# Kernel optimization log

Hardware: AMD Instinct MI355X
Metric: run time of the kernel (lower is better)

Reference implementation:

```python
import jax, jax.numpy as jnp
import numpy as np

N_NODES = 100000
N_EDGES = 400000  # per edge type
N_ETYPES = 3
N_LAYERS = 3      # 1 + (n_layers-1) + 1 with n_layers=2
D = 64


def setup_inputs() -> dict:
    key = jax.random.key(0)
    k1, k2, k3, k4, k5 = jax.random.split(key, 5)
    feat = jax.random.normal(k1, (N_NODES, D), dtype=jnp.float32)
    # SAGEConv weights per (layer, etype): fc_self, fc_neigh, bias
    W_self = jax.random.normal(k2, (N_LAYERS, N_ETYPES, D, D), dtype=jnp.float32) * 0.05
    W_neigh = jax.random.normal(k3, (N_LAYERS, N_ETYPES, D, D), dtype=jnp.float32) * 0.05
    b = jnp.zeros((N_LAYERS, N_ETYPES, D), dtype=jnp.float32)
    src = jax.random.randint(k4, (N_ETYPES, N_EDGES), 0, N_NODES, dtype=jnp.int32)
    dst = jax.random.randint(k5, (N_ETYPES, N_EDGES), 0, N_NODES, dtype=jnp.int32)
    return {"feat": feat, "W_self": W_self, "W_neigh": W_neigh, "b": b,
            "src": src, "dst": dst}


def reference(feat, W_self, W_neigh, b, src, dst):
    # Heterogeneous SAGEConv (mean aggregator) + cross-relation sum, 3 layers.
    N = feat.shape[0]
    L, T = W_self.shape[0], W_self.shape[1]
    E = src.shape[1]
    ones = jnp.ones((E,), dtype=feat.dtype)
    h = feat
    for l in range(L):
        apply_act = l < L - 1  # last layer has no activation
        out = jnp.zeros((N, W_self.shape[-1]), dtype=feat.dtype)
        for t in range(T):  # small fixed set of relation types
            msgs = jnp.take(h, src[t], axis=0)                    # [E, d] gather
            agg = jax.ops.segment_sum(msgs, dst[t], num_segments=N)   # [N, d]
            deg = jax.ops.segment_sum(ones, dst[t], num_segments=N)   # [N]
            mean = agg / jnp.maximum(deg, 1.0)[:, None]           # zero-deg -> 0
            r = h @ W_self[l, t] + mean @ W_neigh[l, t] + b[l, t]
            if apply_act:
                r = jax.nn.relu(r)
            out = out + r  # HeteroGraphConv aggregate='sum'
        h = out
    return h
```

## Files before the change

kernel.cpp:

```cpp
#include <hip/hip_runtime.h>
#include <hip/hip_bf16.h>

#define NN 100000
#define NE 400000
#define NT 3
#define NL 3
#define DD 64
#define M_TOT (NT * NN)
#define RPB 2048
#define NBKT ((M_TOT + RPB - 1) / RPB)
#define P3CAP 32
#define P3GRID 256
#define PCAP 13312
#define CSR_THREADS 1024
#define COLCAP_BKT 9216
#define OVF_CAP 500000


typedef __attribute__((ext_vector_type(8))) short bf16x8;
typedef __attribute__((ext_vector_type(4))) float f32x4;

static __device__ __forceinline__ unsigned short f2b(float f) {
    __hip_bfloat16 b = __float2bfloat16(f);
    return *reinterpret_cast<unsigned short*>(&b);
}
static __device__ __forceinline__ float b2f(unsigned short u) {
    __hip_bfloat16 b = *reinterpret_cast<__hip_bfloat16*>(&u);
    return __bfloat162float(b);
}

__global__ void init_kernel(int* __restrict__ gcur, int* __restrict__ ocnt) {
    int i = threadIdx.x;
    if (i < NBKT) gcur[i] = i * PCAP;
    if (i == 0) ocnt[0] = 0;
}

__global__ __launch_bounds__(256) void pair_scatter(
    const int* __restrict__ src, const int* __restrict__ dst,
    int* __restrict__ gcur, unsigned* __restrict__ pairs,
    uint2* __restrict__ ovf, int* __restrict__ ocnt) {
    __shared__ unsigned buf[NBKT][P3CAP];
    __shared__ int fill[NBKT];
    for (int i = threadIdx.x; i < NBKT; i += 256) fill[i] = 0;
    __syncthreads();
    const int total = NT * NE;
    int per = (total + gridDim.x - 1) / gridDim.x;
    int beg = blockIdx.x * per;
    int fin = beg + per; if (fin > total) fin = total;
    for (int bse = beg; bse < fin; bse += 256) {
        int e = bse + threadIdx.x;
        if (e < fin) {
            int t = e / NE;
            int row = t * NN + dst[e];
            int bk = row >> 11;
            unsigned pr = ((unsigned)(row & 2047) << 17) | (unsigned)src[e];
            int pos = atomicAdd(&fill[bk], 1);
            if (pos < P3CAP) buf[bk][pos] = pr;
            else {
                int o = atomicAdd(ocnt, 1);
                if (o < OVF_CAP) ovf[o] = make_uint2((unsigned)src[e], (unsigned)row);
            }
        }
        __syncthreads();
        for (int bk = threadIdx.x; bk < NBKT; bk += 256) {
            int n = fill[bk]; if (n > P3CAP) n = P3CAP;
            int g = n >> 4;
            if (g) {
                int gb = atomicAdd(&gcur[bk], g * 16);
#pragma unroll
                for (int q = 0; q < 4; ++q)
                    *(int4*)&pairs[gb + q * 4] = *(const int4*)&buf[bk][q * 4];
                if (g == 2)
#pragma unroll
                    for (int q = 0; q < 4; ++q)
                        *(int4*)&pairs[gb + 16 + q * 4] =
                            *(const int4*)&buf[bk][16 + q * 4];
                int rem = n - g * 16;
                for (int k = 0; k < rem; ++k) buf[bk][k] = buf[bk][g * 16 + k];
                fill[bk] = rem;
            } else fill[bk] = n;
        }
        __syncthreads();
    }
    for (int bk = threadIdx.x; bk < NBKT; bk += 256) {
        int n = fill[bk]; if (n > P3CAP) n = P3CAP;
        if (n) {
            int m = (n + 15) & ~15;
            for (int k = n; k < m; ++k) buf[bk][k] = 0xFFFFFFFFu;
            int gb = atomicAdd(&gcur[bk], m);
            for (int grp = 0; grp < m >> 4; ++grp)
#pragma unroll
                for (int q = 0; q < 4; ++q)
                    *(int4*)&pairs[gb + grp * 16 + q * 4] =
                        *(const int4*)&buf[bk][grp * 16 + q * 4];
        }
    }
}

__global__ __launch_bounds__(CSR_THREADS) void bucket_csr(
    const int* __restrict__ gcur, const unsigned* __restrict__ pairs,
    const uint2* __restrict__ ovf, const int* __restrict__ ocnt,
    int* __restrict__ rs, int* __restrict__ rse, int* __restrict__ col) {
    __shared__ int cnt_s[RPB];
    __shared__ int cur_s[RPB];
    __shared__ int part[CSR_THREADS];
    const int bk = blockIdx.x;
    const int row0 = bk * RPB;
    const int nrows = (M_TOT - row0 < RPB) ? (M_TOT - row0) : RPB;
    for (int i = threadIdx.x; i < RPB; i += CSR_THREADS) cnt_s[i] = 0;
    __syncthreads();
    const int pb = bk * PCAP, pe = gcur[bk];
    for (int p = pb + threadIdx.x; p < pe; p += CSR_THREADS) {
        unsigned pr = pairs[p];
        if ((pr & 0x1FFFFu) < NN)
            atomicAdd(&cnt_s[pr >> 17], 1);
    }
    int no = ocnt[0]; if (no > OVF_CAP) no = OVF_CAP;
    for (int o = threadIdx.x; o < no; o += CSR_THREADS) {
        int rl = (int)ovf[o].y - row0;
        if (rl >= 0 && rl < nrows) atomicAdd(&cnt_s[rl], 1);
    }
    __syncthreads();
    int t0 = threadIdx.x * 2, sum = 0;
    int exl[2];
#pragma unroll
    for (int k = 0; k < 2; ++k) { exl[k] = sum; sum += cnt_s[t0 + k]; }
    part[threadIdx.x] = sum;
    __syncthreads();
    for (int o = 1; o < CSR_THREADS; o <<= 1) {
        int v = (threadIdx.x >= o) ? part[threadIdx.x - o] : 0;
        __syncthreads();
        part[threadIdx.x] += v;
        __syncthreads();
    }
    int off = part[threadIdx.x] - sum + bk * COLCAP_BKT;
#pragma unroll
    for (int k = 0; k < 2; ++k) {
        int idx = t0 + k;
        int ex = exl[k] + off;
        cur_s[idx] = ex;
        if (idx < nrows) { rs[row0 + idx] = ex; rse[row0 + idx] = ex + cnt_s[idx]; }
    }
    __syncthreads();
    for (int p = pb + threadIdx.x; p < pe; p += CSR_THREADS) {
        unsigned pr = pairs[p];
        unsigned s = pr & 0x1FFFFu;
        if (s < NN) {
            int pos = atomicAdd(&cur_s[pr >> 17], 1);
            col[pos] = (int)s;
        }
    }
    for (int o = threadIdx.x; o < no; o += CSR_THREADS) {
        int rl = (int)ovf[o].y - row0;
        if (rl >= 0 && rl < nrows) {
            int pos = atomicAdd(&cur_s[rl], 1);
            col[pos] = (int)ovf[o].x;
        }
    }
}

__global__ __launch_bounds__(256) void wtrans_kernel(
    const float* __restrict__ Ws, const float* __restrict__ Wn,
    unsigned short* __restrict__ Wt) {
    int lt = blockIdx.x;
    for (int p = threadIdx.x; p < DD * 2 * DD; p += 256) {
        int j = p >> 7, k = p & 127;
        float v = (k < DD) ? Ws[(size_t)lt * DD * DD + k * DD + j]
                           : Wn[(size_t)lt * DD * DD + (k - DD) * DD + j];
        Wt[(size_t)lt * 8192 + j * 128 + k] = f2b(v);
    }
}

template <int HBF>
__global__ __launch_bounds__(256) void gather_kernel(
    const void* __restrict__ hv, const int* __restrict__ rs,
    const int* __restrict__ rse, const int* __restrict__ col,
    unsigned short* __restrict__ meanb) {
    const int lane = threadIdx.x & 63;
    const int g = lane >> 3;
    const int fc = lane & 7;
    const int i = (blockIdx.x * 4 + (threadIdx.x >> 6)) * 8 + g;
    const bool live = i < M_TOT;
    const int start = live ? rs[i] : 0;
    const int end   = live ? rse[i] : 0;
    const int deg = end - start;
    float acc[8];
#pragma unroll
    for (int j = 0; j < 8; ++j) acc[j] = 0.f;
    const unsigned short* hb = (const unsigned short*)hv;
    const float* hf = (const float*)hv;
    for (int base = 0; base < deg; base += 8) {
        int e = start + base + fc;
        int cl = col[(e < end) ? e : start];

#define GSTEP(K)                                                               \
        {                                                                      \
            int idx = __builtin_amdgcn_ds_swizzle(cl, ((K) << 5) | 24);        \
            bool v = (base + (K)) < deg;                                       \
            float mk = v ? 1.f : 0.f;                                          \
            int ix = v ? idx : 0;                                              \
            if (HBF) {                                                         \
                int4 rv = *(const int4*)&hb[(size_t)ix * DD + fc * 8];         \
                const unsigned* wp = (const unsigned*)&rv;                     \
                _Pragma("unroll")                                              \
                for (int j = 0; j < 4; ++j) {                                  \
                    unsigned w = wp[j];                                        \
                    float lo = __uint_as_float(w << 16);                       \
                    float hi = __uint_as_float(w & 0xffff0000u);               \
                    acc[2 * j]     = fmaf(lo, mk, acc[2 * j]);                 \
                    acc[2 * j + 1] = fmaf(hi, mk, acc[2 * j + 1]);             \
                }                                                              \
            } else {                                                           \
                float4 a = *(const float4*)&hf[(size_t)ix * DD + fc * 8];      \
                float4 b = *(const float4*)&hf[(size_t)ix * DD + fc * 8 + 4];  \
                acc[0] = fmaf(a.x, mk, acc[0]);                                \
                acc[1] = fmaf(a.y, mk, acc[1]);                                \
                acc[2] = fmaf(a.z, mk, acc[2]);                                \
                acc[3] = fmaf(a.w, mk, acc[3]);                                \
                acc[4] = fmaf(b.x, mk, acc[4]);                                \
                acc[5] = fmaf(b.y, mk, acc[5]);                                \
                acc[6] = fmaf(b.z, mk, acc[6]);                                \
                acc[7] = fmaf(b.w, mk, acc[7]);                                \
            }                                                                  \
        }
        GSTEP(0) GSTEP(1) GSTEP(2) GSTEP(3)
        GSTEP(4) GSTEP(5) GSTEP(6) GSTEP(7)
#undef GSTEP
    }
    float sc = (deg > 0) ? 1.f / (float)deg : 0.f;
    unsigned ow[4];
#pragma unroll
    for (int j = 0; j < 4; ++j) {
        unsigned lo = f2b(acc[2 * j] * sc);
        unsigned hi = f2b(acc[2 * j + 1] * sc);
        ow[j] = lo | (hi << 16);
    }
    if (live)
        *(int4*)&meanb[(size_t)i * DD + fc * 8] = *(const int4*)ow;
}

template <int HBF, int OBF>
__global__ __launch_bounds__(256) void layer_gemm(
    const void* __restrict__ hv, const unsigned short* __restrict__ meanb,
    const unsigned short* __restrict__ Wt, const float* __restrict__ bias,
    void* __restrict__ outv, int relu) {
    __shared__ __align__(16) short A_s[64 * 136];
    __shared__ __align__(16) short B_s[64 * 136];

    const int tx = threadIdx.x;
    const int n0 = blockIdx.x * 64;
    const int lane = tx & 63, w = tx >> 6;
    const int q = lane >> 4, m16 = lane & 15;
    const int rr = tx >> 4;
    const int k0 = (tx & 15) * 4;
    const int bj = tx >> 2;
    const int bk = (tx & 3) * 32;

#pragma unroll
    for (int qq = 0; qq < 4; ++qq) {
        int r = rr + 16 * qq;
        int n = n0 + r;
        ushort4 hb4 = make_ushort4(0, 0, 0, 0);
        if (n < NN) {
            if (HBF) {
                hb4 = *(const ushort4*)&((const unsigned short*)hv)[(size_t)n * DD + k0];
            } else {
                float4 hf = *(const float4*)&((const float*)hv)[(size_t)n * DD + k0];
                hb4 = make_ushort4(f2b(hf.x), f2b(hf.y), f2b(hf.z), f2b(hf.w));
            }
        }
        *(ushort4*)&A_s[r * 136 + k0] = hb4;
    }

    float acc_sum[4][4];
#pragma unroll
    for (int c = 0; c < 4; ++c)
#pragma unroll
        for (int r = 0; r < 4; ++r) acc_sum[c][r] = 0.f;

    for (int t = 0; t < NT; ++t) {
#pragma unroll
        for (int qq = 0; qq < 4; ++qq) {
            int r = rr + 16 * qq;
            int n = n0 + r;
            ushort4 mv = make_ushort4(0, 0, 0, 0);
            if (n < NN)
                mv = *(const ushort4*)&meanb[((size_t)t * NN + n) * DD + k0];
            *(ushort4*)&A_s[r * 136 + 64 + k0] = mv;
        }
        {
            const unsigned short* wt = Wt + (size_t)t * 8192 + bj * 128 + bk;
#pragma unroll
            for (int u = 0; u < 4; ++u)
                *(int4*)&B_s[bj * 136 + bk + u * 8] = *(const int4*)&wt[u * 8];
        }
        __syncthreads();

        f32x4 acc[4];
#pragma unroll
        for (int c = 0; c < 4; ++c) acc[c] = (f32x4){0.f, 0.f, 0.f, 0.f};
#pragma unroll
        for (int kt = 0; kt < 4; ++kt) {
            bf16x8 a = *(const bf16x8*)&A_s[(16 * w + m16) * 136 + kt * 32 + q * 8];
#pragma unroll
            for (int c = 0; c < 4; ++c) {
                bf16x8 b = *(const bf16x8*)&B_s[(c * 16 + m16) * 136 + kt * 32 + q * 8];
                acc[c] = __builtin_amdgcn_mfma_f32_16x16x32_bf16(a, b, acc[c], 0, 0, 0);
            }
        }

#pragma unroll
        for (int c = 0; c < 4; ++c) {
            float bv = bias[t * DD + c * 16 + m16];
#pragma unroll
            for (int r = 0; r < 4; ++r) {
                float v = acc[c][r] + bv;
                if (relu) v = fmaxf(v, 0.f);
                acc_sum[c][r] += v;
            }
        }
        __syncthreads();
    }

#pragma unroll
    for (int c = 0; c < 4; ++c)
#pragma unroll
        for (int r = 0; r < 4; ++r) {
            int n = n0 + 16 * w + q * 4 + r;
            if (n >= NN) continue;
            size_t idx = (size_t)n * DD + c * 16 + m16;
            if (OBF)
                ((unsigned short*)outv)[idx] = f2b(acc_sum[c][r]);
            else
                ((float*)outv)[idx] = acc_sum[c][r];
        }
}

extern "C" void kernel_launch(void* const* d_in, const int* in_sizes, int n_in,
                              void* d_out, int out_size, void* d_ws, size_t ws_size,
                              hipStream_t stream) {
    const float* feat    = (const float*)d_in[0];
    const float* W_self  = (const float*)d_in[1];
    const float* W_neigh = (const float*)d_in[2];
    const float* bias    = (const float*)d_in[3];
    const int* src = (const int*)d_in[4];
    const int* dst = (const int*)d_in[5];

    char* ws = (char*)d_ws;
    int* gcur  = (int*)(ws + 0);
    int* ocnt  = (int*)(ws + 1024);
    int* rs    = (int*)(ws + 8192);
    int* rse   = (int*)(ws + 1208320);
    int* col   = (int*)(ws + 2408448);
    unsigned short* Wt    = (unsigned short*)(ws + 7827584);
    unsigned short* X2    = (unsigned short*)(ws + 7975040);
    unsigned short* meanb = (unsigned short*)(ws + 20775040);
    unsigned*       pairs = (unsigned*)(ws + 20775040);
    uint2*          ovf   = (uint2*)(ws + 20775040 + 8388608);

    init_kernel<<<1, 256, 0, stream>>>(gcur, ocnt);
    pair_scatter<<<P3GRID, 256, 0, stream>>>(src, dst, gcur, pairs, ovf, ocnt);
    bucket_csr<<<NBKT, CSR_THREADS, 0, stream>>>(gcur, pairs, ovf, ocnt,
                                                 rs, rse, col);
    wtrans_kernel<<<NL * NT, 256, 0, stream>>>(W_self, W_neigh, Wt);

    unsigned short* X1 = (unsigned short*)d_out;
    const int ggrid = (M_TOT + 31) / 32;
    const int mgrid = (NN + 63) / 64;

    gather_kernel<0><<<ggrid, 256, 0, stream>>>(feat, rs, rse, col, meanb);
    layer_gemm<0, 1><<<mgrid, 256, 0, stream>>>(
        feat, meanb, Wt + 0 * NT * 8192, bias + 0 * NT * DD, X1, 1);
    gather_kernel<1><<<ggrid, 256, 0, stream>>>(X1, rs, rse, col, meanb);
    layer_gemm<1, 1><<<mgrid, 256, 0, stream>>>(
        X1, meanb, Wt + 1 * NT * 8192, bias + 1 * NT * DD, X2, 1);
    gather_kernel<1><<<ggrid, 256, 0, stream>>>(X2, rs, rse, col, meanb);
    layer_gemm<1, 0><<<mgrid, 256, 0, stream>>>(
        X2, meanb, Wt + 2 * NT * 8192, bias + 2 * NT * DD, d_out, 0);
}
```

Measured before the change: 302.9 us.

## Use grid-stride gather with fixed grid and 128-row GEMM tiles

The gather kernel becomes a grid-stride loop over 32-row tiles on a fixed grid of 2048 blocks instead of one block per tile. This cuts block launch and scheduling overhead. The layer GEMM now processes 128 nodes per block, with each wave computing two 16-row M tiles that share each B fragment. This halves the number of weight tile loads into LDS, at the cost of doubling A-tile LDS use and accumulator registers, which may lower occupancy.

```diff
diff --git a/kernel.cpp b/kernel.cpp
--- a/kernel.cpp
+++ b/kernel.cpp
@@ -15,6 +15,7 @@
 #define CSR_THREADS 1024
 #define COLCAP_BKT 9216
 #define OVF_CAP 500000
+#define GGRID 2048
 
 
 typedef __attribute__((ext_vector_type(8))) short bf16x8;
@@ -179,64 +180,67 @@
     const int lane = threadIdx.x & 63;
     const int g = lane >> 3;
     const int fc = lane & 7;
-    const int i = (blockIdx.x * 4 + (threadIdx.x >> 6)) * 8 + g;
-    const bool live = i < M_TOT;
-    const int start = live ? rs[i] : 0;
-    const int end   = live ? rse[i] : 0;
-    const int deg = end - start;
-    float acc[8];
-#pragma unroll
-    for (int j = 0; j < 8; ++j) acc[j] = 0.f;
     const unsigned short* hb = (const unsigned short*)hv;
     const float* hf = (const float*)hv;
-    for (int base = 0; base < deg; base += 8) {
-        int e = start + base + fc;
-        int cl = col[(e < end) ? e : start];
+    const int ntiles = (M_TOT + 31) / 32;
+    for (int tile = blockIdx.x; tile < ntiles; tile += gridDim.x) {
+        const int i = (tile * 4 + (threadIdx.x >> 6)) * 8 + g;
+        const bool live = i < M_TOT;
+        const int start = live ? rs[i] : 0;
+        const int end   = live ? rse[i] : 0;
+        const int deg = end - start;
+        float acc[8];
+#pragma unroll
+        for (int j = 0; j < 8; ++j) acc[j] = 0.f;
+        for (int base = 0; base < deg; base += 8) {
+            int e = start + base + fc;
+            int cl = col[(e < end) ? e : start];
 
 #define GSTEP(K)                                                               \
-        {                                                                      \
-            int idx = __builtin_amdgcn_ds_swizzle(cl, ((K) << 5) | 24);        \
-            bool v = (base + (K)) < deg;                                       \
-            float mk = v ? 1.f : 0.f;                                          \
-            int ix = v ? idx : 0;                                              \
-            if (HBF) {                                                         \
-                int4 rv = *(const int4*)&hb[(size_t)ix * DD + fc * 8];         \
-                const unsigned* wp = (const unsigned*)&rv;                     \
-                _Pragma("unroll")                                              \
-                for (int j = 0; j < 4; ++j) {                                  \
-                    unsigned w = wp[j];                                        \
-                    float lo = __uint_as_float(w << 16);                       \
-                    float hi = __uint_as_float(w & 0xffff0000u);               \
-                    acc[2 * j]     = fmaf(lo, mk, acc[2 * j]);                 \
-                    acc[2 * j + 1] = fmaf(hi, mk, acc[2 * j + 1]);             \
+            {                                                                  \
+                int idx = __builtin_amdgcn_ds_swizzle(cl, ((K) << 5) | 24);    \
+                bool v = (base + (K)) < deg;                                   \
+                float mk = v ? 1.f : 0.f;                                      \
+                int ix = v ? idx : 0;                                          \
+                if (HBF) {                                                     \
+                    int4 rv = *(const int4*)&hb[(size_t)ix * DD + fc * 8];     \
+                    const unsigned* wp = (const unsigned*)&rv;                 \
+                    _Pragma("unroll")                                          \
+                    for (int j = 0; j < 4; ++j) {                              \
+                        unsigned w = wp[j];                                    \
+                        float lo = __uint_as_float(w << 16);                   \
+                        float hi = __uint_as_float(w & 0xffff0000u);           \
+                        acc[2 * j]     = fmaf(lo, mk, acc[2 * j]);             \
+                        acc[2 * j + 1] = fmaf(hi, mk, acc[2 * j + 1]);         \
+                    }                                                          \
+                } else {                                                       \
+                    float4 a = *(const float4*)&hf[(size_t)ix * DD + fc * 8];  \
+                    float4 b = *(const float4*)&hf[(size_t)ix * DD + fc * 8 + 4];\
+                    acc[0] = fmaf(a.x, mk, acc[0]);                            \
+                    acc[1] = fmaf(a.y, mk, acc[1]);                            \
+                    acc[2] = fmaf(a.z, mk, acc[2]);                            \
+                    acc[3] = fmaf(a.w, mk, acc[3]);                            \
+                    acc[4] = fmaf(b.x, mk, acc[4]);                            \
+                    acc[5] = fmaf(b.y, mk, acc[5]);                            \
+                    acc[6] = fmaf(b.z, mk, acc[6]);                            \
+                    acc[7] = fmaf(b.w, mk, acc[7]);                            \
                 }                                                              \
-            } else {                                                           \
-                float4 a = *(const float4*)&hf[(size_t)ix * DD + fc * 8];      \
-                float4 b = *(const float4*)&hf[(size_t)ix * DD + fc * 8 + 4];  \
-                acc[0] = fmaf(a.x, mk, acc[0]);                                \
-                acc[1] = fmaf(a.y, mk, acc[1]);                                \
-                acc[2] = fmaf(a.z, mk, acc[2]);                                \
-                acc[3] = fmaf(a.w, mk, acc[3]);                                \
-                acc[4] = fmaf(b.x, mk, acc[4]);                                \
-                acc[5] = fmaf(b.y, mk, acc[5]);                                \
-                acc[6] = fmaf(b.z, mk, acc[6]);                                \
-                acc[7] = fmaf(b.w, mk, acc[7]);                                \
-            }                                                                  \
-        }
-        GSTEP(0) GSTEP(1) GSTEP(2) GSTEP(3)
-        GSTEP(4) GSTEP(5) GSTEP(6) GSTEP(7)
+            }
+            GSTEP(0) GSTEP(1) GSTEP(2) GSTEP(3)
+            GSTEP(4) GSTEP(5) GSTEP(6) GSTEP(7)
 #undef GSTEP
-    }
-    float sc = (deg > 0) ? 1.f / (float)deg : 0.f;
-    unsigned ow[4];
-#pragma unroll
-    for (int j = 0; j < 4; ++j) {
-        unsigned lo = f2b(acc[2 * j] * sc);
-        unsigned hi = f2b(acc[2 * j + 1] * sc);
-        ow[j] = lo | (hi << 16);
-    }
-    if (live)
-        *(int4*)&meanb[(size_t)i * DD + fc * 8] = *(const int4*)ow;
+        }
+        float sc = (deg > 0) ? 1.f / (float)deg : 0.f;
+        unsigned ow[4];
+#pragma unroll
+        for (int j = 0; j < 4; ++j) {
+            unsigned lo = f2b(acc[2 * j] * sc);
+            unsigned hi = f2b(acc[2 * j + 1] * sc);
+            ow[j] = lo | (hi << 16);
+        }
+        if (live)
+            *(int4*)&meanb[(size_t)i * DD + fc * 8] = *(const int4*)ow;
+    }
 }
 
 template <int HBF, int OBF>
@@ -244,11 +248,11 @@
     const void* __restrict__ hv, const unsigned short* __restrict__ meanb,
     const unsigned short* __restrict__ Wt, const float* __restrict__ bias,
     void* __restrict__ outv, int relu) {
-    __shared__ __align__(16) short A_s[64 * 136];
+    __shared__ __align__(16) short A_s[128 * 136];
     __shared__ __align__(16) short B_s[64 * 136];
 
     const int tx = threadIdx.x;
-    const int n0 = blockIdx.x * 64;
+    const int n0 = blockIdx.x * 128;
     const int lane = tx & 63, w = tx >> 6;
     const int q = lane >> 4, m16 = lane & 15;
     const int rr = tx >> 4;
@@ -257,7 +261,7 @@
     const int bk = (tx & 3) * 32;
 
 #pragma unroll
-    for (int qq = 0; qq < 4; ++qq) {
+    for (int qq = 0; qq < 8; ++qq) {
         int r = rr + 16 * qq;
         int n = n0 + r;
         ushort4 hb4 = make_ushort4(0, 0, 0, 0);
@@ -272,15 +276,17 @@
         *(ushort4*)&A_s[r * 136 + k0] = hb4;
     }
 
-    float acc_sum[4][4];
-#pragma unroll
-    for (int c = 0; c < 4; ++c)
-#pragma unroll
-        for (int r = 0; r < 4; ++r) acc_sum[c][r] = 0.f;
+    float acc_sum[2][4][4];
+#pragma unroll
+    for (int mt = 0; mt < 2; ++mt)
+#pragma unroll
+        for (int c = 0; c < 4; ++c)
+#pragma unroll
+            for (int r = 0; r < 4; ++r) acc_sum[mt][c][r] = 0.f;
 
     for (int t = 0; t < NT; ++t) {
 #pragma unroll
-        for (int qq = 0; qq < 4; ++qq) {
+        for (int qq = 0; qq < 8; ++qq) {
             int r = rr + 16 * qq;
             int n = n0 + r;
             ushort4 mv = make_ushort4(0, 0, 0, 0);
@@ -296,16 +302,20 @@
         }
         __syncthreads();
 
-        f32x4 acc[4];
-#pragma unroll
-        for (int c = 0; c < 4; ++c) acc[c] = (f32x4){0.f, 0.f, 0.f, 0.f};
+        f32x4 acc[2][4];
+#pragma unroll
+        for (int mt = 0; mt < 2; ++mt)
+#pragma unroll
+            for (int c = 0; c < 4; ++c) acc[mt][c] = (f32x4){0.f, 0.f, 0.f, 0.f};
 #pragma unroll
         for (int kt = 0; kt < 4; ++kt) {
-            bf16x8 a = *(const bf16x8*)&A_s[(16 * w + m16) * 136 + kt * 32 + q * 8];
+            bf16x8 a0 = *(const bf16x8*)&A_s[(32 * w + m16) * 136 + kt * 32 + q * 8];
+            bf16x8 a1 = *(const bf16x8*)&A_s[(32 * w + 16 + m16) * 136 + kt * 32 + q * 8];
 #pragma unroll
             for (int c = 0; c < 4; ++c) {
                 bf16x8 b = *(const bf16x8*)&B_s[(c * 16 + m16) * 136 + kt * 32 + q * 8];
-                acc[c] = __builtin_amdgcn_mfma_f32_16x16x32_bf16(a, b, acc[c], 0, 0, 0);
+                acc[0][c] = __builtin_amdgcn_mfma_f32_16x16x32_bf16(a0, b, acc[0][c], 0, 0, 0);
+                acc[1][c] = __builtin_amdgcn_mfma_f32_16x16x32_bf16(a1, b, acc[1][c], 0, 0, 0);
             }
         }
 
@@ -313,27 +323,31 @@
         for (int c = 0; c < 4; ++c) {
             float bv = bias[t * DD + c * 16 + m16];
 #pragma unroll
+            for (int mt = 0; mt < 2; ++mt)
+#pragma unroll
+                for (int r = 0; r < 4; ++r) {
+                    float v = acc[mt][c][r] + bv;
+                    if (relu) v = fmaxf(v, 0.f);
+                    acc_sum[mt][c][r] += v;
+                }
+        }
+        __syncthreads();
+    }
+
+#pragma unroll
+    for (int mt = 0; mt < 2; ++mt)
+#pragma unroll
+        for (int c = 0; c < 4; ++c)
+#pragma unroll
             for (int r = 0; r < 4; ++r) {
-                float v = acc[c][r] + bv;
-                if (relu) v = fmaxf(v, 0.f);
-                acc_sum[c][r] += v;
-            }
-        }
-        __syncthreads();
-    }
-
-#pragma unroll
-    for (int c = 0; c < 4; ++c)
-#pragma unroll
-        for (int r = 0; r < 4; ++r) {
-            int n = n0 + 16 * w + q * 4 + r;
-            if (n >= NN) continue;
-            size_t idx = (size_t)n * DD + c * 16 + m16;
-            if (OBF)
-                ((unsigned short*)outv)[idx] = f2b(acc_sum[c][r]);
-            else
-                ((float*)outv)[idx] = acc_sum[c][r];
-        }
+                int n = n0 + 32 * w + 16 * mt + q * 4 + r;
+                if (n >= NN) continue;
+                size_t idx = (size_t)n * DD + c * 16 + m16;
+                if (OBF)
+                    ((unsigned short*)outv)[idx] = f2b(acc_sum[mt][c][r]);
+                else
+                    ((float*)outv)[idx] = acc_sum[mt][c][r];
+            }
 }
 
 extern "C" void kernel_launch(void* const* d_in, const int* in_sizes, int n_in,
@@ -365,16 +379,15 @@
     wtrans_kernel<<<NL * NT, 256, 0, stream>>>(W_self, W_neigh, Wt);
 
     unsigned short* X1 = (unsigned short*)d_out;
-    const int ggrid = (M_TOT + 31) / 32;
-    const int mgrid = (NN + 63) / 64;
-
-    gather_kernel<0><<<ggrid, 256, 0, stream>>>(feat, rs, rse, col, meanb);
+    const int mgrid = (NN + 127) / 128;
+
+    gather_kernel<0><<<GGRID, 256, 0, stream>>>(feat, rs, rse, col, meanb);
     layer_gemm<0, 1><<<mgrid, 256, 0, stream>>>(
         feat, meanb, Wt + 0 * NT * 8192, bias + 0 * NT * DD, X1, 1);
-    gather_kernel<1><<<ggrid, 256, 0, stream>>>(X1, rs, rse, col, meanb);
+    gather_kernel<1><<<GGRID, 256, 0, stream>>>(X1, rs, rse, col, meanb);
     layer_gemm<1, 1><<<mgrid, 256, 0, stream>>>(
         X1, meanb, Wt + 1 * NT * 8192, bias + 1 * NT * DD, X2, 1);
-    gather_kernel<1><<<ggrid, 256, 0, stream>>>(X2, rs, rse, col, meanb);
+    gather_kernel<1><<<GGRID, 256, 0, stream>>>(X2, rs, rse, col, meanb);
     layer_gemm<1, 0><<<mgrid, 256, 0, stream>>>(
         X2, meanb, Wt + 2 * NT * 8192, bias + 2 * NT * DD, d_out, 0);
 }
```

After: 336.9 us. +11.2%, slower.
